# Optimization experiments

Hardware: AMD Instinct MI355X
Metric: run time of the kernel (lower is better)

## Reference

```python
import jax, jax.numpy as jnp
import numpy as np

IN_F, OUT_F, RANK = 4096, 4096, 1024
B, S = 4, 2048


def soft_threshold24(w):
    """Soft-threshold 2:4 sparsification along the last dim.
    For each group of 4, the two smallest-magnitude entries are zeroed and the
    kept entries are shrunk by the threshold (2nd-smallest magnitude)."""
    g = w.reshape(-1, 4)
    m = jnp.abs(g)
    t = jnp.sort(m, axis=-1)[:, 1:2]  # largest pruned magnitude per group
    sp = jnp.sign(g) * jnp.maximum(m - t, 0.0)
    return sp.reshape(w.shape)


def fake_fp8_mm(a, b):
    """FP8-simulated GEMM: fp16 operands, fp32 accumulate/output (matches fake_fp8_mm)."""
    return jnp.matmul(a.astype(jnp.float16), b.astype(jnp.float16),
                      preferred_element_type=jnp.float32)


def setup_inputs() -> dict:
    key = jax.random.key(0)
    k1, k2, k3 = jax.random.split(key, 3)
    x = jax.random.normal(k1, (B, S, IN_F), dtype=jnp.float32)
    std_a = (2.0 / (IN_F + RANK)) ** 0.5   # xavier_normal for (in_features, rank)
    std_b = (2.0 / (OUT_F + RANK)) ** 0.5  # xavier_normal for (out_features, rank)
    weight_A = jax.random.normal(k2, (IN_F, RANK), dtype=jnp.float32) * std_a
    weight_B = jax.random.normal(k3, (OUT_F, RANK), dtype=jnp.float32) * std_b
    bias = jnp.zeros((OUT_F,), dtype=jnp.float32)
    scale_A = jnp.ones((), dtype=jnp.float32)  # sparse_init_scale buffer
    scale_B = jnp.ones((), dtype=jnp.float32)
    return {"x": x, "weight_A": weight_A, "weight_B": weight_B, "bias": bias,
            "scale_A": scale_A, "scale_B": scale_B}


def reference(x, weight_A, weight_B, bias, scale_A, scale_B):
    # sparse low-rank factors
    wa = soft_threshold24(weight_A) * scale_A  # (in, rank)
    wb = soft_threshold24(weight_B) * scale_B  # (out, rank)
    lead = x.shape[:-1]
    xf = x.reshape(-1, x.shape[-1])            # (T, in)
    x_proj = fake_fp8_mm(xf, wa)               # (T, rank) == x @ A_sparse
    out = fake_fp8_mm(x_proj, wb.T) + bias     # (T, out) == x_proj @ B_sparse^T + b
    return out.reshape(*lead, OUT_F)
```

## Files before the change

kernel.cpp:

```cpp
#include <hip/hip_runtime.h>

#define IN_FEAT 4096
#define OUT_FEAT 4096
#define RANK 1024
#define TOK 8192

typedef _Float16 f16x8 __attribute__((ext_vector_type(8)));
typedef _Float16 f16x4 __attribute__((ext_vector_type(4)));
typedef float f32x4 __attribute__((ext_vector_type(4)));

#define GLD_LDS16(g, l)                                                         \
  __builtin_amdgcn_global_load_lds(                                             \
      (__attribute__((address_space(1))) const void*)(g),                       \
      (__attribute__((address_space(3))) void*)(l), 16, 0, 0)

#define MIDBAR()                                        \
  __builtin_amdgcn_s_barrier();                         \
  asm volatile("s_waitcnt lgkmcnt(0)" ::: "memory")
#define ENDBAR() __builtin_amdgcn_s_barrier()


__device__ __forceinline__ void soft24(const float4 g, float s,
                                       float& r0, float& r1, float& r2, float& r3) {
  const float m0 = fabsf(g.x), m1 = fabsf(g.y), m2 = fabsf(g.z), m3 = fabsf(g.w);
  const float lo1 = fminf(m0, m1), hi1 = fmaxf(m0, m1);
  const float lo2 = fminf(m2, m3), hi2 = fmaxf(m2, m3);
  const float t = fminf(fmaxf(lo1, lo2), fminf(hi1, hi2));
  r0 = copysignf(fmaxf(m0 - t, 0.0f), g.x) * s;
  r1 = copysignf(fmaxf(m1 - t, 0.0f), g.y) * s;
  r2 = copysignf(fmaxf(m2 - t, 0.0f), g.z) * s;
  r3 = copysignf(fmaxf(m3 - t, 0.0f), g.w) * s;
}

__global__ __launch_bounds__(256) void sparsify_A_kernel(
    const float* __restrict__ wA, const float* __restrict__ scaleA,
    _Float16* __restrict__ waT) {
  const int idx = blockIdx.x * 256 + threadIdx.x;
  const int i = idx & (IN_FEAT - 1);
  const int jg = idx >> 12;
  const float4 g = *reinterpret_cast<const float4*>(wA + (size_t)i * RANK + jg * 4);
  const float s = scaleA[0];
  float r0, r1, r2, r3;
  soft24(g, s, r0, r1, r2, r3);
  const size_t base = (size_t)(jg * 4) * IN_FEAT + i;
  waT[base] = (_Float16)r0;
  waT[base + IN_FEAT] = (_Float16)r1;
  waT[base + 2 * IN_FEAT] = (_Float16)r2;
  waT[base + 3 * IN_FEAT] = (_Float16)r3;
}

__global__ __launch_bounds__(256) void sparsify_B_kernel(
    const float* __restrict__ wB, const float* __restrict__ scaleB,
    _Float16* __restrict__ wbs) {
  const int idx = blockIdx.x * 256 + threadIdx.x;
  const float4 g = *reinterpret_cast<const float4*>(wB + (size_t)idx * 4);
  const float s = scaleB[0];
  float r0, r1, r2, r3;
  soft24(g, s, r0, r1, r2, r3);
  f16x4 h;
  h[0] = (_Float16)r0; h[1] = (_Float16)r1; h[2] = (_Float16)r2; h[3] = (_Float16)r3;
  *reinterpret_cast<f16x4*>(wbs + (size_t)idx * 4) = h;
}

__global__ __launch_bounds__(256) void cast_x_kernel(
    const float* __restrict__ x, _Float16* __restrict__ x16) {
  const size_t i = ((size_t)blockIdx.x * 256 + threadIdx.x) * 8;
  const float4 f0 = *reinterpret_cast<const float4*>(x + i);
  const float4 f1 = *reinterpret_cast<const float4*>(x + i + 4);
  f16x8 h;
  h[0] = (_Float16)f0.x; h[1] = (_Float16)f0.y;
  h[2] = (_Float16)f0.z; h[3] = (_Float16)f0.w;
  h[4] = (_Float16)f1.x; h[5] = (_Float16)f1.y;
  h[6] = (_Float16)f1.z; h[7] = (_Float16)f1.w;
  *reinterpret_cast<f16x8*>(x16 + i) = h;
}

template <int N, int K, bool A_F32, bool OUT_F16>
__global__ __launch_bounds__(256, 4) void gemm128(
    const void* __restrict__ Av, const _Float16* __restrict__ Bh,
    void* __restrict__ Cv, const float* __restrict__ bias) {
  __shared__ __attribute__((aligned(128))) char lds[32768];
  char* ldsA = lds;
  char* ldsB = lds + 16384;

  const int tid = threadIdx.x;
  const int lane = tid & 63;
  const int w = tid >> 6;
  const int wrow = (w >> 1) * 64;
  const int wcol = (w & 1) * 64;

  constexpr int GX = N / 128;
  const int nwg = GX * (TOK / 128);
  const int l = blockIdx.y * GX + blockIdx.x;
  const int wg = (l & 7) * (nwg >> 3) + (l >> 3);
  const int brow = (wg / GX) * 128;
  const int bcol = (wg % GX) * 128;

  f32x4 acc[4][4] = {};

  for (int k0 = 0; k0 < K; k0 += 64) {
    __syncthreads();
#pragma unroll
    for (int it = 0; it < 4; ++it) {
      const int c = it * 256 + tid;
      const int row = c >> 3;
      const int u = c & 7;
      const _Float16* gsrc =
          Bh + (size_t)(bcol + row) * K + k0 + ((u ^ (row & 7)) << 3);
      GLD_LDS16(gsrc, ldsB + c * 16);
    }
    if constexpr (A_F32) {
      const float* Af = (const float*)Av;
#pragma unroll
      for (int it = 0; it < 4; ++it) {
        const int c = it * 256 + tid;
        const int row = c >> 3;
        const int u = c & 7;
        const float* gsrc = Af + (size_t)(brow + row) * K + k0 + (u << 3);
        const float4 f0 = *reinterpret_cast<const float4*>(gsrc);
        const float4 f1 = *reinterpret_cast<const float4*>(gsrc + 4);
        f16x8 h;
        h[0] = (_Float16)f0.x; h[1] = (_Float16)f0.y;
        h[2] = (_Float16)f0.z; h[3] = (_Float16)f0.w;
        h[4] = (_Float16)f1.x; h[5] = (_Float16)f1.y;
        h[6] = (_Float16)f1.z; h[7] = (_Float16)f1.w;
        *reinterpret_cast<f16x8*>(ldsA + row * 128 + ((u ^ (row & 7)) << 4)) = h;
      }
    } else {
      const _Float16* Ah = (const _Float16*)Av;
#pragma unroll
      for (int it = 0; it < 4; ++it) {
        const int c = it * 256 + tid;
        const int row = c >> 3;
        const int u = c & 7;
        const _Float16* gsrc =
            Ah + (size_t)(brow + row) * K + k0 + ((u ^ (row & 7)) << 3);
        GLD_LDS16(gsrc, ldsA + c * 16);
      }
    }
    __syncthreads();
#pragma unroll
    for (int kk = 0; kk < 2; ++kk) {
      f16x8 af[4], bf[4];
#pragma unroll
      for (int m = 0; m < 4; ++m) {
        const int row = wrow + m * 16 + (lane & 15);
        const int u = (kk * 4 + (lane >> 4)) ^ (row & 7);
        af[m] = *reinterpret_cast<const f16x8*>(ldsA + row * 128 + u * 16);
      }
#pragma unroll
      for (int n = 0; n < 4; ++n) {
        const int row = wcol + n * 16 + (lane & 15);
        const int u = (kk * 4 + (lane >> 4)) ^ (row & 7);
        bf[n] = *reinterpret_cast<const f16x8*>(ldsB + row * 128 + u * 16);
      }
#pragma unroll
      for (int m = 0; m < 4; ++m)
#pragma unroll
        for (int n = 0; n < 4; ++n)
          acc[m][n] =
              __builtin_amdgcn_mfma_f32_16x16x32_f16(af[m], bf[n], acc[m][n], 0, 0, 0);
    }
  }

  const int r4 = (lane >> 4) * 4;
  const int cl = lane & 15;
  if constexpr (OUT_F16) {
    _Float16* C = (_Float16*)Cv;
#pragma unroll
    for (int m = 0; m < 4; ++m)
#pragma unroll
      for (int n = 0; n < 4; ++n)
#pragma unroll
        for (int j = 0; j < 4; ++j) {
          const int rr = brow + wrow + m * 16 + r4 + j;
          const int cc = bcol + wcol + n * 16 + cl;
          C[(size_t)rr * N + cc] = (_Float16)acc[m][n][j];
        }
  } else {
    float* C = (float*)Cv;
#pragma unroll
    for (int n = 0; n < 4; ++n) {
      const int cc = bcol + wcol + n * 16 + cl;
      const float bv = bias[cc];
#pragma unroll
      for (int m = 0; m < 4; ++m)
#pragma unroll
        for (int j = 0; j < 4; ++j) {
          const int rr = brow + wrow + m * 16 + r4 + j;
          C[(size_t)rr * N + cc] = acc[m][n][j] + bv;
        }
    }
  }
}

template <int M, int N, int K>
__global__ __launch_bounds__(512, 2) void gemm1_k(
    const _Float16* __restrict__ A, const _Float16* __restrict__ B,
    _Float16* __restrict__ C) {
  extern __shared__ char lds[];

  const int tid = threadIdx.x;
  const int lane = tid & 63;
  const int w = tid >> 6;
  const int wr = w >> 2;
  const int wc = w & 3;
  const int l15 = lane & 15;
  const int ubase = lane >> 4;

  constexpr int GX = N / 256;
  constexpr int NWG = GX * (M / 128);
  const int l = blockIdx.y * GX + blockIdx.x;
  const int wg = (l & 7) * (NWG >> 3) + (l >> 3);
  const int brow = (wg / GX) * 128;
  const int bcol = (wg % GX) * 256;

  f32x4 acc[4][4] = {};
  f16x8 af[4][2], bf01[2][2], bf23[2][2];

  auto lda = [&](int slot) {
#pragma unroll
    for (int i = 0; i < 4; ++i)
#pragma unroll
      for (int ks = 0; ks < 2; ++ks) {
        const int row = wr * 64 + i * 16 + l15;
        const int u = (ks * 4 + ubase) ^ (row & 7);
        af[i][ks] =
            *reinterpret_cast<const f16x8*>(lds + slot * 16384 + row * 128 + u * 16);
      }
  };
  auto ldb = [&](int slot, int nbase, f16x8 (*dst)[2]) {
#pragma unroll
    for (int j = 0; j < 2; ++j)
#pragma unroll
      for (int ks = 0; ks < 2; ++ks) {
        const int row = wc * 64 + (nbase + j) * 16 + l15;
        const int u = (ks * 4 + ubase) ^ (row & 7);
        dst[j][ks] = *reinterpret_cast<const f16x8*>(lds + 32768 + slot * 32768 +
                                                     row * 128 + u * 16);
      }
  };
  auto stageA = [&](int kof, int slot) {
#pragma unroll
    for (int r = 0; r < 2; ++r) {
      const int c = r * 512 + tid;
      const int row = c >> 3;
      const int u = c & 7;
      GLD_LDS16(A + (size_t)(brow + row) * K + kof + ((u ^ (row & 7)) << 3),
                lds + slot * 16384 + c * 16);
    }
  };
  auto stageB = [&](int kof, int slot) {
#pragma unroll
    for (int r = 0; r < 4; ++r) {
      const int c = r * 512 + tid;
      const int row = c >> 3;
      const int u = c & 7;
      GLD_LDS16(B + (size_t)(bcol + row) * K + kof + ((u ^ (row & 7)) << 3),
                lds + 32768 + slot * 32768 + c * 16);
    }
  };

#define QUAD16(BF, NO)                                                         \
  __builtin_amdgcn_s_setprio(1);                                               \
  _Pragma("unroll") for (int ks = 0; ks < 2; ++ks)                             \
  _Pragma("unroll") for (int i = 0; i < 4; ++i)                                \
  _Pragma("unroll") for (int j = 0; j < 2; ++j)                                \
      acc[i][(NO) + j] = __builtin_amdgcn_mfma_f32_16x16x32_f16(               \
          af[i][ks], BF[j][ks], acc[i][(NO) + j], 0, 0, 0);                    \
  __builtin_amdgcn_s_setprio(0);

  constexpr int NT = K / 64;

  stageA(0, 0);
  stageB(0, 0);
  stageA(64, 1);
  asm volatile("s_waitcnt vmcnt(2)" ::: "memory");
  __builtin_amdgcn_s_barrier();

  for (int tt = 0; tt < NT; tt += 2) {
    const bool lastI = (tt + 2 >= NT);
    const int kB1 = tt * 64 + 64;
    const int kAB2 = tt * 64 + 128;
    const int kA3 = tt * 64 + 192;

    lda(0);
    ldb(0, 0, bf01);
    stageB(kB1, 1);
    MIDBAR();
    QUAD16(bf01, 0);
    ENDBAR();
    ldb(0, 2, bf23);
    if (!lastI) {
      stageA(kAB2, 0);
      asm volatile("s_waitcnt vmcnt(2)" ::: "memory");
    } else {
      asm volatile("s_waitcnt vmcnt(0)" ::: "memory");
    }
    MIDBAR();
    QUAD16(bf23, 2);
    ENDBAR();
    lda(1);
    ldb(1, 0, bf01);
    if (!lastI) stageB(kAB2, 0);
    MIDBAR();
    QUAD16(bf01, 0);
    ENDBAR();
    ldb(1, 2, bf23);
    if (!lastI) {
      stageA(kA3, 1);
      asm volatile("s_waitcnt vmcnt(2)" ::: "memory");
    }
    MIDBAR();
    QUAD16(bf23, 2);
    ENDBAR();
  }

  const int r4 = (lane >> 4) * 4;
#pragma unroll
  for (int m = 0; m < 4; ++m)
#pragma unroll
    for (int n = 0; n < 4; ++n)
#pragma unroll
      for (int j = 0; j < 4; ++j) {
        const int rr = brow + wr * 64 + m * 16 + r4 + j;
        const int cc = bcol + wc * 64 + n * 16 + l15;
        C[(size_t)rr * N + cc] = (_Float16)acc[m][n][j];
      }
#undef QUAD16
}

#define AOFF(s, h) (((s) * 2 + (h)) * 16384)
#define BOFF(s, h) (65536 + ((s) * 2 + (h)) * 16384)

#define QUAD(AF, BF, MO, NO)                                                   \
  __builtin_amdgcn_s_setprio(1);                                               \
  _Pragma("unroll") for (int ks = 0; ks < 2; ++ks)                             \
  _Pragma("unroll") for (int i = 0; i < 4; ++i)                                \
  _Pragma("unroll") for (int j = 0; j < 2; ++j)                                \
      acc[(MO) + i][(NO) + j] = __builtin_amdgcn_mfma_f32_16x16x32_f16(        \
          AF[i][ks], BF[j][ks], acc[(MO) + i][(NO) + j], 0, 0, 0);             \
  __builtin_amdgcn_s_setprio(0);

template <int M, int N, int K>
__global__ __launch_bounds__(512, 2) void gemm256(
    const _Float16* __restrict__ A, const _Float16* __restrict__ B,
    float* __restrict__ C, const float* __restrict__ bias) {
  extern __shared__ char lds[];

  const int tid = threadIdx.x;
  const int lane = tid & 63;
  const int w = tid >> 6;
  const int wr = w >> 2;
  const int wc = w & 3;
  const int l15 = lane & 15;
  const int ubase = lane >> 4;

  constexpr int GX = N / 256;
  constexpr int NWG = GX * (M / 256);
  const int l = blockIdx.y * GX + blockIdx.x;
  const int wg = (l & 7) * (NWG >> 3) + (l >> 3);
  const int brow = (wg / GX) * 256;
  const int bcol = (wg % GX) * 256;

  const _Float16* Abase = A + (size_t)brow * K;
  const _Float16* Bbase = B + (size_t)bcol * K;

  auto stage = [&](const _Float16* srcBase, int rowOff, int kof, int ldsOff) {
#pragma unroll
    for (int r = 0; r < 2; ++r) {
      const int c = r * 512 + tid;
      const int row = c >> 3;
      const int u = c & 7;
      const _Float16* g =
          srcBase + (size_t)(rowOff + row) * K + kof + ((u ^ (row & 7)) << 3);
      GLD_LDS16(g, lds + ldsOff + c * 16);
    }
  };

  f32x4 acc[8][4] = {};
  f16x8 af[4][2], bf01[2][2], bf23[2][2];

#define LDA_GRP(SLOT, MBASE)                                                   \
  _Pragma("unroll") for (int i = 0; i < 4; ++i)                                \
  _Pragma("unroll") for (int ks = 0; ks < 2; ++ks) {                           \
    const int row = ((MBASE) + i) * 16 + l15;                                  \
    const int u = (ks * 4 + ubase) ^ (row & 7);                                \
    af[i][ks] = *reinterpret_cast<const f16x8*>(                               \
        lds + AOFF(SLOT, wr) + row * 128 + u * 16);                            \
  }
#define LDB_GRP(SLOT, NBASE, DST)                                              \
  _Pragma("unroll") for (int j = 0; j < 2; ++j)                                \
  _Pragma("unroll") for (int ks = 0; ks < 2; ++ks) {                           \
    const int row = (wc & 1) * 64 + ((NBASE) + j) * 16 + l15;                  \
    const int u = (ks * 4 + ubase) ^ (row & 7);                                \
    DST[j][ks] = *reinterpret_cast<const f16x8*>(                              \
        lds + BOFF(SLOT, wc >> 1) + row * 128 + u * 16);                       \
  }

  constexpr int NT = K / 64;

  stage(Abase, 0, 0, AOFF(0, 0));
  stage(Abase, 128, 0, AOFF(0, 1));
  stage(Bbase, 0, 0, BOFF(0, 0));
  stage(Bbase, 128, 0, BOFF(0, 1));
  stage(Bbase, 0, 64, BOFF(1, 0));
  stage(Bbase, 128, 64, BOFF(1, 1));
  asm volatile("s_waitcnt vmcnt(4)" ::: "memory");
  __builtin_amdgcn_s_barrier();

  for (int tt = 0; tt < NT; tt += 2) {
    const bool last = (tt + 2 >= NT);
    const int kof1 = tt * 64 + 64;
    const int kof2 = tt * 64 + 128;
    const int kof3 = tt * 64 + 192;

    LDA_GRP(0, 0);
    LDB_GRP(0, 0, bf01);
    stage(Abase, 0, kof1, AOFF(1, 0));
    MIDBAR();
    QUAD(af, bf01, 0, 0);
    ENDBAR();

    LDB_GRP(0, 2, bf23);
    stage(Abase, 128, kof1, AOFF(1, 1));
    MIDBAR();
    QUAD(af, bf23, 0, 2);
    ENDBAR();

    LDA_GRP(0, 4);
    if (!last) stage(Bbase, 0, kof2, BOFF(0, 0));
    MIDBAR();
    QUAD(af, bf01, 4, 0);
    ENDBAR();

    if (!last) {
      stage(Bbase, 128, kof2, BOFF(0, 1));
      asm volatile("s_waitcnt vmcnt(4)" ::: "memory");
    } else {
      asm volatile("s_waitcnt vmcnt(0)" ::: "memory");
    }
    MIDBAR();
    QUAD(af, bf23, 4, 2);
    ENDBAR();

    LDA_GRP(1, 0);
    LDB_GRP(1, 0, bf01);
    if (!last) stage(Abase, 0, kof2, AOFF(0, 0));
    MIDBAR();
    QUAD(af, bf01, 0, 0);
    ENDBAR();

    LDB_GRP(1, 2, bf23);
    if (!last) stage(Abase, 128, kof2, AOFF(0, 1));
    MIDBAR();
    QUAD(af, bf23, 0, 2);
    ENDBAR();

    LDA_GRP(1, 4);
    if (!last) stage(Bbase, 0, kof3, BOFF(1, 0));
    MIDBAR();
    QUAD(af, bf01, 4, 0);
    ENDBAR();

    if (!last) {
      stage(Bbase, 128, kof3, BOFF(1, 1));
      asm volatile("s_waitcnt vmcnt(4)" ::: "memory");
    }
    MIDBAR();
    QUAD(af, bf23, 4, 2);
    ENDBAR();
  }

  const int r4 = (lane >> 4) * 4;
#pragma unroll
  for (int n = 0; n < 4; ++n) {
    const int cc = bcol + wc * 64 + n * 16 + l15;
    const float bv = bias[cc];
#pragma unroll
    for (int m = 0; m < 8; ++m)
#pragma unroll
      for (int j = 0; j < 4; ++j) {
        const int rr = brow + wr * 128 + m * 16 + r4 + j;
        C[(size_t)rr * N + cc] = acc[m][n][j] + bv;
      }
  }
}


extern "C" void kernel_launch(void* const* d_in, const int* in_sizes, int n_in,
                              void* d_out, int out_size, void* d_ws, size_t ws_size,
                              hipStream_t stream) {
  const float* x = (const float*)d_in[0];
  const float* wA = (const float*)d_in[1];
  const float* wB = (const float*)d_in[2];
  const float* bias = (const float*)d_in[3];
  const float* scaleA = (const float*)d_in[4];
  const float* scaleB = (const float*)d_in[5];
  float* out = (float*)d_out;

  char* ws = (char*)d_ws;
  _Float16* waT = (_Float16*)ws;
  _Float16* wbs = (_Float16*)(ws + (size_t)RANK * IN_FEAT * 2);
  _Float16* xp =
      (_Float16*)(ws + (size_t)RANK * IN_FEAT * 2 + (size_t)OUT_FEAT * RANK * 2);
  _Float16* x16 = (_Float16*)(ws + (size_t)RANK * IN_FEAT * 2 +
                              (size_t)OUT_FEAT * RANK * 2 + (size_t)TOK * RANK * 2);
  const size_t needed = (size_t)RANK * IN_FEAT * 2 + (size_t)OUT_FEAT * RANK * 2 +
                        (size_t)TOK * RANK * 2 + (size_t)TOK * IN_FEAT * 2;

  hipLaunchKernelGGL(sparsify_A_kernel, dim3((IN_FEAT * RANK / 4) / 256), dim3(256),
                     0, stream, wA, scaleA, waT);
  hipLaunchKernelGGL(sparsify_B_kernel, dim3((OUT_FEAT * RANK / 4) / 256), dim3(256),
                     0, stream, wB, scaleB, wbs);

  if (ws_size >= needed) {
    hipLaunchKernelGGL(cast_x_kernel, dim3((TOK * IN_FEAT / 8) / 256), dim3(256),
                       0, stream, x, x16);
    (void)hipFuncSetAttribute(
        reinterpret_cast<const void*>(&gemm1_k<TOK, RANK, IN_FEAT>),
        hipFuncAttributeMaxDynamicSharedMemorySize, 98304);
    hipLaunchKernelGGL((gemm1_k<TOK, RANK, IN_FEAT>),
                       dim3(RANK / 256, TOK / 128), dim3(512), 98304, stream,
                       x16, waT, xp);
  } else {
    hipLaunchKernelGGL((gemm128<RANK, IN_FEAT, true, true>),
                       dim3(RANK / 128, TOK / 128), dim3(256), 0, stream,
                       (const void*)x, waT, (void*)xp, nullptr);
  }

  (void)hipFuncSetAttribute(
      reinterpret_cast<const void*>(&gemm256<TOK, OUT_FEAT, RANK>),
      hipFuncAttributeMaxDynamicSharedMemorySize, 131072);
  hipLaunchKernelGGL((gemm256<TOK, OUT_FEAT, RANK>),
                     dim3(OUT_FEAT / 256, TOK / 256), dim3(512), 131072, stream,
                     xp, wbs, out, bias);
}
```

Baseline: 204.5 us.

## Triple-buffer GEMM1, merge MFMA phases, swap operands for vectorized epilogue stores

```diff
diff --git a/kernel.cpp b/kernel.cpp
--- a/kernel.cpp
+++ b/kernel.cpp
@@ -195,7 +195,7 @@
 }
 
 template <int M, int N, int K>
-__global__ __launch_bounds__(512, 2) void gemm1_k(
+__global__ __launch_bounds__(512, 2) void gemm1_m(
     const _Float16* __restrict__ A, const _Float16* __restrict__ B,
     _Float16* __restrict__ C) {
   extern __shared__ char lds[];
@@ -216,9 +216,40 @@
   const int bcol = (wg % GX) * 256;
 
   f32x4 acc[4][4] = {};
-  f16x8 af[4][2], bf01[2][2], bf23[2][2];
-
-  auto lda = [&](int slot) {
+  f16x8 af[4][2], bf[4][2];
+
+  auto stageA = [&](int kof, int slot) {
+#pragma unroll
+    for (int r = 0; r < 2; ++r) {
+      const int c = r * 512 + tid;
+      const int row = c >> 3;
+      const int u = c & 7;
+      GLD_LDS16(A + (size_t)(brow + row) * K + kof + ((u ^ (row & 7)) << 3),
+                lds + slot * 16384 + c * 16);
+    }
+  };
+  auto stageB = [&](int kof, int slot) {
+#pragma unroll
+    for (int r = 0; r < 4; ++r) {
+      const int c = r * 512 + tid;
+      const int row = c >> 3;
+      const int u = c & 7;
+      GLD_LDS16(B + (size_t)(bcol + row) * K + kof + ((u ^ (row & 7)) << 3),
+                lds + 49152 + slot * 32768 + c * 16);
+    }
+  };
+
+  constexpr int NT = K / 64;
+
+  stageA(0, 0);
+  stageB(0, 0);
+  stageA(64, 1);
+  stageB(64, 1);
+  asm volatile("s_waitcnt vmcnt(6)" ::: "memory");
+  __builtin_amdgcn_s_barrier();
+
+  int slot = 0;
+  for (int t = 0; t < NT; ++t) {
 #pragma unroll
     for (int i = 0; i < 4; ++i)
 #pragma unroll
@@ -228,122 +259,59 @@
         af[i][ks] =
             *reinterpret_cast<const f16x8*>(lds + slot * 16384 + row * 128 + u * 16);
       }
-  };
-  auto ldb = [&](int slot, int nbase, f16x8 (*dst)[2]) {
-#pragma unroll
-    for (int j = 0; j < 2; ++j)
+#pragma unroll
+    for (int j = 0; j < 4; ++j)
 #pragma unroll
       for (int ks = 0; ks < 2; ++ks) {
-        const int row = wc * 64 + (nbase + j) * 16 + l15;
+        const int row = wc * 64 + j * 16 + l15;
         const int u = (ks * 4 + ubase) ^ (row & 7);
-        dst[j][ks] = *reinterpret_cast<const f16x8*>(lds + 32768 + slot * 32768 +
-                                                     row * 128 + u * 16);
+        bf[j][ks] = *reinterpret_cast<const f16x8*>(lds + 49152 + slot * 32768 +
+                                                    row * 128 + u * 16);
       }
-  };
-  auto stageA = [&](int kof, int slot) {
-#pragma unroll
-    for (int r = 0; r < 2; ++r) {
-      const int c = r * 512 + tid;
-      const int row = c >> 3;
-      const int u = c & 7;
-      GLD_LDS16(A + (size_t)(brow + row) * K + kof + ((u ^ (row & 7)) << 3),
-                lds + slot * 16384 + c * 16);
-    }
-  };
-  auto stageB = [&](int kof, int slot) {
-#pragma unroll
-    for (int r = 0; r < 4; ++r) {
-      const int c = r * 512 + tid;
-      const int row = c >> 3;
-      const int u = c & 7;
-      GLD_LDS16(B + (size_t)(bcol + row) * K + kof + ((u ^ (row & 7)) << 3),
-                lds + 32768 + slot * 32768 + c * 16);
-    }
-  };
-
-#define QUAD16(BF, NO)                                                         \
-  __builtin_amdgcn_s_setprio(1);                                               \
-  _Pragma("unroll") for (int ks = 0; ks < 2; ++ks)                             \
-  _Pragma("unroll") for (int i = 0; i < 4; ++i)                                \
-  _Pragma("unroll") for (int j = 0; j < 2; ++j)                                \
-      acc[i][(NO) + j] = __builtin_amdgcn_mfma_f32_16x16x32_f16(               \
-          af[i][ks], BF[j][ks], acc[i][(NO) + j], 0, 0, 0);                    \
-  __builtin_amdgcn_s_setprio(0);
-
-  constexpr int NT = K / 64;
-
-  stageA(0, 0);
-  stageB(0, 0);
-  stageA(64, 1);
-  asm volatile("s_waitcnt vmcnt(2)" ::: "memory");
-  __builtin_amdgcn_s_barrier();
-
-  for (int tt = 0; tt < NT; tt += 2) {
-    const bool lastI = (tt + 2 >= NT);
-    const int kB1 = tt * 64 + 64;
-    const int kAB2 = tt * 64 + 128;
-    const int kA3 = tt * 64 + 192;
-
-    lda(0);
-    ldb(0, 0, bf01);
-    stageB(kB1, 1);
+    if (t + 2 < NT) {
+      int s2 = slot + 2;
+      if (s2 >= 3) s2 -= 3;
+      stageA((t + 2) * 64, s2);
+      stageB((t + 2) * 64, s2);
+      asm volatile("s_waitcnt vmcnt(6)" ::: "memory");
+    } else if (t + 2 == NT) {
+      asm volatile("s_waitcnt vmcnt(0)" ::: "memory");
+    }
     MIDBAR();
-    QUAD16(bf01, 0);
+    __builtin_amdgcn_s_setprio(1);
+#pragma unroll
+    for (int ks = 0; ks < 2; ++ks)
+#pragma unroll
+      for (int i = 0; i < 4; ++i)
+#pragma unroll
+        for (int j = 0; j < 4; ++j)
+          acc[i][j] = __builtin_amdgcn_mfma_f32_16x16x32_f16(
+              bf[j][ks], af[i][ks], acc[i][j], 0, 0, 0);
+    __builtin_amdgcn_s_setprio(0);
     ENDBAR();
-    ldb(0, 2, bf23);
-    if (!lastI) {
-      stageA(kAB2, 0);
-      asm volatile("s_waitcnt vmcnt(2)" ::: "memory");
-    } else {
-      asm volatile("s_waitcnt vmcnt(0)" ::: "memory");
-    }
-    MIDBAR();
-    QUAD16(bf23, 2);
-    ENDBAR();
-    lda(1);
-    ldb(1, 0, bf01);
-    if (!lastI) stageB(kAB2, 0);
-    MIDBAR();
-    QUAD16(bf01, 0);
-    ENDBAR();
-    ldb(1, 2, bf23);
-    if (!lastI) {
-      stageA(kA3, 1);
-      asm volatile("s_waitcnt vmcnt(2)" ::: "memory");
-    }
-    MIDBAR();
-    QUAD16(bf23, 2);
-    ENDBAR();
+    ++slot;
+    if (slot == 3) slot = 0;
   }
 
   const int r4 = (lane >> 4) * 4;
 #pragma unroll
   for (int m = 0; m < 4; ++m)
 #pragma unroll
-    for (int n = 0; n < 4; ++n)
-#pragma unroll
-      for (int j = 0; j < 4; ++j) {
-        const int rr = brow + wr * 64 + m * 16 + r4 + j;
-        const int cc = bcol + wc * 64 + n * 16 + l15;
-        C[(size_t)rr * N + cc] = (_Float16)acc[m][n][j];
-      }
-#undef QUAD16
+    for (int n = 0; n < 4; ++n) {
+      const int rr = brow + wr * 64 + m * 16 + l15;
+      const int cc = bcol + wc * 64 + n * 16 + r4;
+      f16x4 h;
+#pragma unroll
+      for (int j = 0; j < 4; ++j) h[j] = (_Float16)acc[m][n][j];
+      *reinterpret_cast<f16x4*>(C + (size_t)rr * N + cc) = h;
+    }
 }
 
 #define AOFF(s, h) (((s) * 2 + (h)) * 16384)
 #define BOFF(s, h) (65536 + ((s) * 2 + (h)) * 16384)
 
-#define QUAD(AF, BF, MO, NO)                                                   \
-  __builtin_amdgcn_s_setprio(1);                                               \
-  _Pragma("unroll") for (int ks = 0; ks < 2; ++ks)                             \
-  _Pragma("unroll") for (int i = 0; i < 4; ++i)                                \
-  _Pragma("unroll") for (int j = 0; j < 2; ++j)                                \
-      acc[(MO) + i][(NO) + j] = __builtin_amdgcn_mfma_f32_16x16x32_f16(        \
-          AF[i][ks], BF[j][ks], acc[(MO) + i][(NO) + j], 0, 0, 0);             \
-  __builtin_amdgcn_s_setprio(0);
-
 template <int M, int N, int K>
-__global__ __launch_bounds__(512, 2) void gemm256(
+__global__ __launch_bounds__(512, 2) void gemm2_m(
     const _Float16* __restrict__ A, const _Float16* __restrict__ B,
     float* __restrict__ C, const float* __restrict__ bias) {
   extern __shared__ char lds[];
@@ -397,6 +365,18 @@
     DST[j][ks] = *reinterpret_cast<const f16x8*>(                              \
         lds + BOFF(SLOT, wc >> 1) + row * 128 + u * 16);                       \
   }
+
+#define MFMA32(MO)                                                             \
+  __builtin_amdgcn_s_setprio(1);                                               \
+  _Pragma("unroll") for (int ks = 0; ks < 2; ++ks)                             \
+  _Pragma("unroll") for (int i = 0; i < 4; ++i)                                \
+  _Pragma("unroll") for (int j = 0; j < 2; ++j) {                              \
+    acc[(MO) + i][j] = __builtin_amdgcn_mfma_f32_16x16x32_f16(                 \
+        bf01[j][ks], af[i][ks], acc[(MO) + i][j], 0, 0, 0);                    \
+    acc[(MO) + i][2 + j] = __builtin_amdgcn_mfma_f32_16x16x32_f16(             \
+        bf23[j][ks], af[i][ks], acc[(MO) + i][2 + j], 0, 0, 0);                \
+  }                                                                            \
+  __builtin_amdgcn_s_setprio(0);
 
   constexpr int NT = K / 64;
 
@@ -417,73 +397,58 @@
 
     LDA_GRP(0, 0);
     LDB_GRP(0, 0, bf01);
+    LDB_GRP(0, 2, bf23);
     stage(Abase, 0, kof1, AOFF(1, 0));
-    MIDBAR();
-    QUAD(af, bf01, 0, 0);
-    ENDBAR();
-
-    LDB_GRP(0, 2, bf23);
     stage(Abase, 128, kof1, AOFF(1, 1));
     MIDBAR();
-    QUAD(af, bf23, 0, 2);
+    MFMA32(0);
     ENDBAR();
 
     LDA_GRP(0, 4);
-    if (!last) stage(Bbase, 0, kof2, BOFF(0, 0));
-    MIDBAR();
-    QUAD(af, bf01, 4, 0);
-    ENDBAR();
-
     if (!last) {
+      stage(Bbase, 0, kof2, BOFF(0, 0));
       stage(Bbase, 128, kof2, BOFF(0, 1));
       asm volatile("s_waitcnt vmcnt(4)" ::: "memory");
     } else {
       asm volatile("s_waitcnt vmcnt(0)" ::: "memory");
     }
     MIDBAR();
-    QUAD(af, bf23, 4, 2);
+    MFMA32(4);
     ENDBAR();
 
     LDA_GRP(1, 0);
     LDB_GRP(1, 0, bf01);
-    if (!last) stage(Abase, 0, kof2, AOFF(0, 0));
+    LDB_GRP(1, 2, bf23);
+    if (!last) {
+      stage(Abase, 0, kof2, AOFF(0, 0));
+      stage(Abase, 128, kof2, AOFF(0, 1));
+    }
     MIDBAR();
-    QUAD(af, bf01, 0, 0);
+    MFMA32(0);
     ENDBAR();
 
-    LDB_GRP(1, 2, bf23);
-    if (!last) stage(Abase, 128, kof2, AOFF(0, 1));
-    MIDBAR();
-    QUAD(af, bf23, 0, 2);
-    ENDBAR();
-
     LDA_GRP(1, 4);
-    if (!last) stage(Bbase, 0, kof3, BOFF(1, 0));
-    MIDBAR();
-    QUAD(af, bf01, 4, 0);
-    ENDBAR();
-
     if (!last) {
+      stage(Bbase, 0, kof3, BOFF(1, 0));
       stage(Bbase, 128, kof3, BOFF(1, 1));
       asm volatile("s_waitcnt vmcnt(4)" ::: "memory");
     }
     MIDBAR();
-    QUAD(af, bf23, 4, 2);
+    MFMA32(4);
     ENDBAR();
   }
 
   const int r4 = (lane >> 4) * 4;
 #pragma unroll
   for (int n = 0; n < 4; ++n) {
-    const int cc = bcol + wc * 64 + n * 16 + l15;
-    const float bv = bias[cc];
-#pragma unroll
-    for (int m = 0; m < 8; ++m)
-#pragma unroll
-      for (int j = 0; j < 4; ++j) {
-        const int rr = brow + wr * 128 + m * 16 + r4 + j;
-        C[(size_t)rr * N + cc] = acc[m][n][j] + bv;
-      }
+    const int cc = bcol + wc * 64 + n * 16 + r4;
+    const f32x4 bv = *reinterpret_cast<const f32x4*>(bias + cc);
+#pragma unroll
+    for (int m = 0; m < 8; ++m) {
+      const int rr = brow + wr * 128 + m * 16 + l15;
+      f32x4 o = acc[m][n] + bv;
+      *reinterpret_cast<f32x4*>(C + (size_t)rr * N + cc) = o;
+    }
   }
 }
 
@@ -518,10 +483,10 @@
     hipLaunchKernelGGL(cast_x_kernel, dim3((TOK * IN_FEAT / 8) / 256), dim3(256),
                        0, stream, x, x16);
     (void)hipFuncSetAttribute(
-        reinterpret_cast<const void*>(&gemm1_k<TOK, RANK, IN_FEAT>),
-        hipFuncAttributeMaxDynamicSharedMemorySize, 98304);
-    hipLaunchKernelGGL((gemm1_k<TOK, RANK, IN_FEAT>),
-                       dim3(RANK / 256, TOK / 128), dim3(512), 98304, stream,
+        reinterpret_cast<const void*>(&gemm1_m<TOK, RANK, IN_FEAT>),
+        hipFuncAttributeMaxDynamicSharedMemorySize, 147456);
+    hipLaunchKernelGGL((gemm1_m<TOK, RANK, IN_FEAT>),
+                       dim3(RANK / 256, TOK / 128), dim3(512), 147456, stream,
                        x16, waT, xp);
   } else {
     hipLaunchKernelGGL((gemm128<RANK, IN_FEAT, true, true>),
@@ -530,9 +495,9 @@
   }
 
   (void)hipFuncSetAttribute(
-      reinterpret_cast<const void*>(&gemm256<TOK, OUT_FEAT, RANK>),
+      reinterpret_cast<const void*>(&gemm2_m<TOK, OUT_FEAT, RANK>),
       hipFuncAttributeMaxDynamicSharedMemorySize, 131072);
-  hipLaunchKernelGGL((gemm256<TOK, OUT_FEAT, RANK>),
+  hipLaunchKernelGGL((gemm2_m<TOK, OUT_FEAT, RANK>),
                      dim3(OUT_FEAT / 256, TOK / 256), dim3(512), 131072, stream,
                      xp, wbs, out, bias);
 }
```

After: 204.8 us. Within noise of the previous version (+0.1%).
